# Optimization experiments

Measured on AMD Instinct MI355X. Metric: run time of the kernel, lower is better.

Reference implementation:

```python
import jax, jax.numpy as jnp
import numpy as np

NUM_CLASSES = 2
BG_PID = 5532
NUM_ROIS = 128          # cfg.TRAIN.BATCH_SIZE
NUM_FG_MAX = 32         # round(cfg.TRAIN.FG_FRACTION * BATCH_SIZE), FG_FRACTION = 0.25
FG_THRESH = 0.5
BG_THRESH_HI = 0.5
BG_THRESH_LO = 0.1
MEANS = jnp.array([0.0, 0.0, 0.0, 0.0], dtype=jnp.float32)
STDS = jnp.array([0.1, 0.1, 0.2, 0.2], dtype=jnp.float32)
INSIDE_W = jnp.array([1.0, 1.0, 1.0, 1.0], dtype=jnp.float32)


def _make_boxes(key, n, img_w=1000.0, img_h=600.0):
    k1, k2, k3, k4 = jax.random.split(key, 4)
    x1 = jax.random.uniform(k1, (n,)) * (img_w - 330.0)
    y1 = jax.random.uniform(k2, (n,)) * (img_h - 350.0)
    w = 20.0 + jax.random.uniform(k3, (n,)) * 300.0
    h = 40.0 + jax.random.uniform(k4, (n,)) * 300.0
    return jnp.stack([x1, y1, x1 + w, y1 + h], axis=1).astype(jnp.float32)


def setup_inputs() -> dict:
    key = jax.random.key(0)
    kr, kg, kp = jax.random.split(key, 3)
    R, G = 131072, 256
    rois = _make_boxes(kr, R)
    all_rois = jnp.concatenate([jnp.zeros((R, 1), jnp.float32), rois], axis=1)  # [R,5]
    gtb = _make_boxes(kg, G)
    labels = jnp.ones((G, 1), jnp.float32)  # person class = 1
    pids = jax.random.randint(kp, (G, 1), 0, BG_PID).astype(jnp.float32)
    gt_boxes = jnp.concatenate([gtb, labels, pids], axis=1)  # [G,6]
    return {"all_rois": all_rois, "gt_boxes": gt_boxes}


def bbox_overlaps(a, b):
    iw = jnp.minimum(a[:, None, 2], b[None, :, 2]) - jnp.maximum(a[:, None, 0], b[None, :, 0]) + 1.0
    ih = jnp.minimum(a[:, None, 3], b[None, :, 3]) - jnp.maximum(a[:, None, 1], b[None, :, 1]) + 1.0
    iw = jnp.maximum(iw, 0.0)
    ih = jnp.maximum(ih, 0.0)
    area_a = (a[:, 2] - a[:, 0] + 1.0) * (a[:, 3] - a[:, 1] + 1.0)
    area_b = (b[:, 2] - b[:, 0] + 1.0) * (b[:, 3] - b[:, 1] + 1.0)
    inter = iw * ih
    return inter / (area_a[:, None] + area_b[None, :] - inter)


def bbox_transform(ex, gt):
    ew = ex[:, 2] - ex[:, 0] + 1.0
    eh = ex[:, 3] - ex[:, 1] + 1.0
    ecx = ex[:, 0] + 0.5 * ew
    ecy = ex[:, 1] + 0.5 * eh
    gw = gt[:, 2] - gt[:, 0] + 1.0
    gh = gt[:, 3] - gt[:, 1] + 1.0
    gcx = gt[:, 0] + 0.5 * gw
    gcy = gt[:, 1] + 0.5 * gh
    return jnp.stack([(gcx - ecx) / ew, (gcy - ecy) / eh,
                      jnp.log(gw / ew), jnp.log(gh / eh)], axis=1)


def _forward(all_rois, gt_boxes):
    G = gt_boxes.shape[0]
    gt_rois = jnp.concatenate([jnp.zeros((G, 1), all_rois.dtype), gt_boxes[:, :4]], axis=1)
    rois_all = jnp.concatenate([all_rois, gt_rois], axis=0)  # [R+G,5]
    N = rois_all.shape[0]
    overlaps = bbox_overlaps(rois_all[:, 1:5], gt_boxes[:, :4])  # [R+G, G]
    argmax_ov = jnp.argmax(overlaps, axis=1)
    max_ov = jnp.max(overlaps, axis=1)
    labels_all = gt_boxes[argmax_ov, 4]
    pids_all = gt_boxes[argmax_ov, 5]
    fg_mask = max_ov >= FG_THRESH
    bg_mask = (max_ov < BG_THRESH_HI) & (max_ov >= BG_THRESH_LO)
    num_fg = jnp.minimum(jnp.int32(NUM_FG_MAX), fg_mask.sum().astype(jnp.int32))
    num_bg = jnp.minimum(jnp.int32(NUM_ROIS) - num_fg, bg_mask.sum().astype(jnp.int32))
    # deterministic 'take first k' selection (DEBUG path of the original),
    # expressed as a fixed-shape scatter: rank within fg/bg -> output slot
    fg_rank = (jnp.cumsum(fg_mask) - 1).astype(jnp.int32)
    bg_rank = (jnp.cumsum(bg_mask) - 1).astype(jnp.int32)
    idx = jnp.arange(N, dtype=jnp.int32)
    pos_fg = jnp.where(fg_mask & (fg_rank < num_fg), fg_rank, jnp.int32(NUM_ROIS))
    pos_bg = jnp.where(bg_mask & (bg_rank < num_bg), num_fg + bg_rank, jnp.int32(NUM_ROIS))
    keep = jnp.zeros((NUM_ROIS,), jnp.int32)
    keep = keep.at[pos_fg].set(idx, mode="drop")
    keep = keep.at[pos_bg].set(idx, mode="drop")
    slot_is_fg = jnp.arange(NUM_ROIS) < num_fg
    rois = rois_all[keep]                                   # [128,5]
    labels = jnp.where(slot_is_fg, labels_all[keep], 0.0)
    pids = jnp.where(slot_is_fg, pids_all[keep], jnp.float32(BG_PID))
    tgt = bbox_transform(rois[:, 1:5], gt_boxes[argmax_ov[keep], :4])
    tgt = (tgt - MEANS) / STDS
    cls = jnp.round(labels).astype(jnp.int32)
    onehot = jax.nn.one_hot(cls, NUM_CLASSES, dtype=tgt.dtype) * (labels > 0).astype(tgt.dtype)[:, None]
    bbox_targets = (onehot[:, :, None] * tgt[:, None, :]).reshape(NUM_ROIS, 4 * NUM_CLASSES)
    bbox_inside = (onehot[:, :, None] * INSIDE_W[None, None, :]).reshape(NUM_ROIS, 4 * NUM_CLASSES)
    bbox_outside = (onehot[:, :, None] * jnp.ones((4,), tgt.dtype)).reshape(NUM_ROIS, 4 * NUM_CLASSES)
    return rois, labels, pids, bbox_targets, bbox_inside, bbox_outside


def reference(all_rois, gt_boxes):
    rois, labels, pids, bt, bi, bo = _forward(all_rois, gt_boxes)
    return rois, labels.astype(jnp.int32), pids.astype(jnp.int32), bt, bi, bo
```

## Files before the change

kernel.cpp:

```cpp
#include <hip/hip_runtime.h>
#include <stdint.h>

#define OUT_ROIS 128
#define FG_MAX 32
#define BG_PID_F 5532.0f
#define MAXCH 2304


__global__ __launch_bounds__(256, 4) void ptl_classify(
    const float* __restrict__ all_rois, const float* __restrict__ gt,
    int R, int G, int N,
    ulonglong2* __restrict__ mb2)
{
#pragma clang fp contract(off)
    __shared__ float4 g4[256];
    __shared__ float  gA[256];
    __shared__ uint8_t flg[4][128];
    const int t = threadIdx.x;
    const int w = t >> 6, lane = t & 63;

    if (t < G) {
        const float* p = gt + (size_t)t * 6;
        const float a = p[0], b = p[1], c = p[2], d = p[3];
        g4[t] = make_float4(a, b, c, d);
        gA[t] = ((c - a) + 1.0f) * ((d - b) + 1.0f);
    }
    __syncthreads();

    const int base = blockIdx.x * 128;
    float x1a, y1a, x2a, y2a, x1b, y1b, x2b, y2b;
    {
        const int i0 = base + lane;
        if (i0 < N) {
            if (i0 < R) { const float* p = all_rois + (size_t)i0 * 5; x1a=p[1]; y1a=p[2]; x2a=p[3]; y2a=p[4]; }
            else        { const float* p = gt + (size_t)(i0 - R) * 6; x1a=p[0]; y1a=p[1]; x2a=p[2]; y2a=p[3]; }
        } else { x1a=0.0f; y1a=0.0f; x2a=-2.0f; y2a=-2.0f; }
        const int i1 = base + 64 + lane;
        if (i1 < N) {
            if (i1 < R) { const float* p = all_rois + (size_t)i1 * 5; x1b=p[1]; y1b=p[2]; x2b=p[3]; y2b=p[4]; }
            else        { const float* p = gt + (size_t)(i1 - R) * 6; x1b=p[0]; y1b=p[1]; x2b=p[2]; y2b=p[3]; }
        } else { x1b=0.0f; y1b=0.0f; x2b=-2.0f; y2b=-2.0f; }
    }
    const float Aa = ((x2a - x1a) + 1.0f) * ((y2a - y1a) + 1.0f);
    const float Ab = ((x2b - x1b) + 1.0f) * ((y2b - y1b) + 1.0f);

    float aF0 = -1e38f, aB0 = -1e38f, aF1 = -1e38f, aB1 = -1e38f;

#define IOU2(QQ, GAv)                                                   \
    do {                                                                \
        const float4 q_ = (QQ); const float ga_ = (GAv);                \
        {   float iw = (fminf(x2a, q_.z) - fmaxf(x1a, q_.x)) + 1.0f;    \
            float ih = (fminf(y2a, q_.w) - fmaxf(y1a, q_.y)) + 1.0f;    \
            iw = fmaxf(iw, 0.0f); ih = fmaxf(ih, 0.0f);                 \
            const float I = iw * ih;                                    \
            const float D = (Aa + ga_) - I;                             \
            const float h  = fmaf(-0.5f, D, I);                         \
            const float gF = fmaf(0x1p-26f, D, h);                      \
            const float h2 = fmaf(-0.1f, D, I);                         \
            const float gB = fmaf(0x1p-28f, D, h2);                     \
            aF0 = fmaxf(aF0, gF); aB0 = fmaxf(aB0, gB); }               \
        {   float iw = (fminf(x2b, q_.z) - fmaxf(x1b, q_.x)) + 1.0f;    \
            float ih = (fminf(y2b, q_.w) - fmaxf(y1b, q_.y)) + 1.0f;    \
            iw = fmaxf(iw, 0.0f); ih = fmaxf(ih, 0.0f);                 \
            const float I = iw * ih;                                    \
            const float D = (Ab + ga_) - I;                             \
            const float h  = fmaf(-0.5f, D, I);                         \
            const float gF = fmaf(0x1p-26f, D, h);                      \
            const float h2 = fmaf(-0.1f, D, I);                         \
            const float gB = fmaf(0x1p-28f, D, h2);                     \
            aF1 = fmaxf(aF1, gF); aB1 = fmaxf(aB1, gB); }               \
    } while (0)

    if (G == 256) {
        const int jbeg = w * 64;
        float4 qb0[8], qb1[8];
        float  ga0[8], ga1[8];
#pragma unroll
        for (int uu = 0; uu < 8; ++uu) { qb0[uu] = g4[jbeg + uu]; ga0[uu] = gA[jbeg + uu]; }
#pragma unroll
        for (int grp = 0; grp < 8; ++grp) {
            if ((grp & 1) == 0) {
                if (grp + 1 < 8) {
#pragma unroll
                    for (int uu = 0; uu < 8; ++uu) {
                        qb1[uu] = g4[jbeg + (grp + 1) * 8 + uu];
                        ga1[uu] = gA[jbeg + (grp + 1) * 8 + uu];
                    }
                }
#pragma unroll
                for (int uu = 0; uu < 8; ++uu) IOU2(qb0[uu], ga0[uu]);
            } else {
                if (grp + 1 < 8) {
#pragma unroll
                    for (int uu = 0; uu < 8; ++uu) {
                        qb0[uu] = g4[jbeg + (grp + 1) * 8 + uu];
                        ga0[uu] = gA[jbeg + (grp + 1) * 8 + uu];
                    }
                }
#pragma unroll
                for (int uu = 0; uu < 8; ++uu) IOU2(qb1[uu], ga1[uu]);
            }
        }
    } else {
        const int jbeg = (G * w) >> 2, jend = (G * (w + 1)) >> 2;
        for (int j = jbeg; j < jend; ++j) IOU2(g4[j], gA[j]);
    }
#undef IOU2

    flg[w][lane]      = (uint8_t)((aF0 >= 0.0f ? 1u : 0u) | (aB0 > 0.0f ? 2u : 0u));
    flg[w][64 + lane] = (uint8_t)((aF1 >= 0.0f ? 1u : 0u) | (aB1 > 0.0f ? 2u : 0u));
    __syncthreads();

    if (t < 128) {
        const uint32_t u = (uint32_t)flg[0][t] | flg[1][t] | flg[2][t] | flg[3][t];
        const int i2 = base + t;
        int cls = (u & 1u) ? 1 : ((u & 2u) ? 2 : 0);
        if (i2 >= N) cls = 0;
        unsigned long long mF = __ballot(cls == 1);
        unsigned long long mB = __ballot(cls == 2);
        if ((t & 63) == 0) {
            ulonglong2 v; v.x = mF; v.y = mB;
            mb2[blockIdx.x * 2 + (t >> 6)] = v;
        }
    }
}

__global__ __launch_bounds__(256) void ptl_select_emit(
    const float* __restrict__ all_rois, const float* __restrict__ gt,
    const ulonglong2* __restrict__ mb2,
    int R, int G, int N, int nch,
    float* __restrict__ out)
{
#pragma clang fp contract(off)
    __shared__ int sF[MAXCH], sB[MAXCH];
    __shared__ int tsF[256], tsB[256];
    __shared__ int keep[OUT_ROIS];
    __shared__ int sam[OUT_ROIS];
    __shared__ int nwork;
    __shared__ uint32_t work[256];
    __shared__ float4 g4s[256];
    __shared__ float  gAs[256];
    const int t = threadIdx.x;

    if (t < G) {
        const float* p = gt + (size_t)t * 6;
        const float a = p[0], b = p[1], c = p[2], d = p[3];
        g4s[t] = make_float4(a, b, c, d);
        gAs[t] = ((c - a) + 1.0f) * ((d - b) + 1.0f);
    }
    for (int c = t; c < MAXCH; c += 256) {
        if (c < nch) {
            const ulonglong2 v = mb2[c];
            sF[c] = __popcll(v.x); sB[c] = __popcll(v.y);
        } else { sF[c] = 0; sB[c] = 0; }
    }
    if (t < OUT_ROIS) { keep[t] = 0; sam[t] = 0; }
    if (t == 0) nwork = 0;
    __syncthreads();

    const int c0 = t * (MAXCH / 256);
    int baseF = 0, baseB = 0;
#pragma unroll
    for (int k = 0; k < MAXCH / 256; ++k) { baseF += sF[c0 + k]; baseB += sB[c0 + k]; }
    tsF[t] = baseF; tsB[t] = baseB;
    __syncthreads();
    for (int d = 1; d < 256; d <<= 1) {
        int vF = (t >= d) ? tsF[t - d] : 0;
        int vB = (t >= d) ? tsB[t - d] : 0;
        __syncthreads();
        tsF[t] += vF; tsB[t] += vB;
        __syncthreads();
    }
    const int tf = tsF[255], tb = tsB[255];
    const int num_fg = tf < FG_MAX ? tf : FG_MAX;
    const int rem = OUT_ROIS - num_fg;
    const int num_bg = tb < rem ? tb : rem;

    int rF = tsF[t] - baseF, rB = tsB[t] - baseB;
#pragma unroll
    for (int k = 0; k < MAXCH / 256; ++k) {
        const int c = c0 + k;
        const int cf = sF[c], cb = sB[c];
        const bool need = ((cf > 0 && rF < num_fg) || (cb > 0 && rB < num_bg)) && (c < nch);
        if (need) {
            const uint32_t efc = (uint32_t)(rF < 255 ? rF : 255);
            const uint32_t ebc = (uint32_t)(rB < 255 ? rB : 255);
            const int p = atomicAdd(&nwork, 1);
            work[p] = ((uint32_t)c << 16) | (efc << 8) | ebc;
        }
        rF += cf; rB += cb;
    }
    __syncthreads();

    const int nw = nwork;
    for (int idx = t; idx < nw; idx += 256) {
        const uint32_t e = work[idx];
        const int c = (int)(e >> 16);
        const ulonglong2 v = mb2[c];
        unsigned long long m = v.x;
        int off = (int)((e >> 8) & 0xFF);
        while (m) {
            const int b = __builtin_ctzll(m);
            m &= m - 1;
            if (off < num_fg) keep[off] = c * 64 + b;
            ++off;
        }
        m = v.y;
        off = (int)(e & 0xFF);
        while (m) {
            const int b = __builtin_ctzll(m);
            m &= m - 1;
            if (off < num_bg) keep[num_fg + off] = c * 64 + b;
            ++off;
        }
    }
    __syncthreads();

    {
        const int grp = t >> 3, l8 = t & 7;
        if (grp < num_fg) {
            const int k = keep[grp];
            float x1, y1, x2, y2;
            if (k < R) { const float* p = all_rois + (size_t)k * 5; x1=p[1]; y1=p[2]; x2=p[3]; y2=p[4]; }
            else       { const float* p = gt + (size_t)(k - R) * 6; x1=p[0]; y1=p[1]; x2=p[2]; y2=p[3]; }
            const float A = ((x2 - x1) + 1.0f) * ((y2 - y1) + 1.0f);
            float mv = -1.0f; int mj = 0;
            for (int j = l8; j < G; j += 8) {
                const float4 q = g4s[j];
                const float ga = gAs[j];
                float iw = (fminf(x2, q.z) - fmaxf(x1, q.x)) + 1.0f;
                float ih = (fminf(y2, q.w) - fmaxf(y1, q.y)) + 1.0f;
                iw = fmaxf(iw, 0.0f); ih = fmaxf(ih, 0.0f);
                const float inter = iw * ih;
                const float iou = inter / ((A + ga) - inter);
                if (iou > mv) { mv = iou; mj = j; }
            }
#pragma unroll
            for (int m = 1; m < 8; m <<= 1) {
                const float ov = __shfl_xor(mv, m);
                const int oj = __shfl_xor(mj, m);
                if (ov > mv || (ov == mv && oj < mj)) { mv = ov; mj = oj; }
            }
            if (l8 == 0) sam[grp] = mj;
        }
    }
    __syncthreads();

    if (t < OUT_ROIS) {
        const int s = t;
        const int k = keep[s];
        const bool isfg = s < num_fg;
        float x1, y1, x2, y2;
        if (k < R) { const float* p = all_rois + (size_t)k * 5; x1=p[1]; y1=p[2]; x2=p[3]; y2=p[4]; }
        else       { const float* p = gt + (size_t)(k - R) * 6; x1=p[0]; y1=p[1]; x2=p[2]; y2=p[3]; }
        const int amax = sam[s];
        const float* g = gt + (size_t)amax * 6;
        const float gx1v = g[0], gy1v = g[1], gx2v = g[2], gy2v = g[3];
        const float label = isfg ? g[4] : 0.0f;
        const float pid = isfg ? g[5] : BG_PID_F;

        float* ro = out + (size_t)s * 5;
        ro[0] = 0.0f; ro[1] = x1; ro[2] = y1; ro[3] = x2; ro[4] = y2;
        out[640 + s] = (float)(int)label;
        out[768 + s] = (float)(int)pid;

        const float ew = (x2 - x1) + 1.0f, eh = (y2 - y1) + 1.0f;
        const float ecx = x1 + 0.5f * ew, ecy = y1 + 0.5f * eh;
        const float gw = (gx2v - gx1v) + 1.0f, gh = (gy2v - gy1v) + 1.0f;
        const float gcx = gx1v + 0.5f * gw, gcy = gy1v + 0.5f * gh;
        float tv[4];
        tv[0] = ((gcx - ecx) / ew) / 0.1f;
        tv[1] = ((gcy - ecy) / eh) / 0.1f;
        tv[2] = logf(gw / ew) / 0.2f;
        tv[3] = logf(gh / eh) / 0.2f;

        const int cls = (int)roundf(label);
        const float on = (label > 0.0f) ? 1.0f : 0.0f;

        float* bt = out + 896  + (size_t)s * 8;
        float* bi = out + 1920 + (size_t)s * 8;
        float* bo = out + 2944 + (size_t)s * 8;
#pragma unroll
        for (int cc = 0; cc < 2; ++cc) {
            const float sel = (cc == cls) ? on : 0.0f;
#pragma unroll
            for (int j = 0; j < 4; ++j) {
                bt[cc * 4 + j] = sel * tv[j];
                bi[cc * 4 + j] = sel;
                bo[cc * 4 + j] = sel;
            }
        }
    }
}

extern "C" void kernel_launch(void* const* d_in, const int* in_sizes, int n_in,
                              void* d_out, int out_size, void* d_ws, size_t ws_size,
                              hipStream_t stream) {
    const float* all_rois = (const float*)d_in[0];
    const float* gt       = (const float*)d_in[1];
    const int R = in_sizes[0] / 5;
    const int G = in_sizes[1] / 6;
    const int N = R + G;
    const int nblk = (N + 127) / 128;
    const int nch = (N + 63) / 64;

    ulonglong2* mb2 = (ulonglong2*)d_ws;
    float* out = (float*)d_out;

    ptl_classify<<<nblk, 256, 0, stream>>>(all_rois, gt, R, G, N, mb2);
    ptl_select_emit<<<1, 256, 0, stream>>>(all_rois, gt, mb2, R, G, N, nch, out);
}
```

Measured before the change: 38.74 us.

## Replace shared-memory block scan with register wave-shuffle scan; recompute gt areas inline

The select kernel now keeps per-thread chunk popcounts in registers and computes the prefix sum with wave-level shuffle-up scans plus a four-entry cross-wave combine, replacing the shared-memory staging and the Hillis-Steele block scan that needed many __syncthreads. The classify kernel drops the shared gt-area array and recomputes each gt box area inline from the float4, trading extra ALU work in the hot IoU loop for fewer LDS loads and less shared memory. The inline area is computed in the same order as before, so results should match bitwise.

```diff
diff --git a/kernel.cpp b/kernel.cpp
--- a/kernel.cpp
+++ b/kernel.cpp
@@ -5,6 +5,7 @@
 #define FG_MAX 32
 #define BG_PID_F 5532.0f
 #define MAXCH 2304
+#define CPT 9
 
 
 __global__ __launch_bounds__(256, 4) void ptl_classify(
@@ -14,16 +15,13 @@
 {
 #pragma clang fp contract(off)
     __shared__ float4 g4[256];
-    __shared__ float  gA[256];
     __shared__ uint8_t flg[4][128];
     const int t = threadIdx.x;
     const int w = t >> 6, lane = t & 63;
 
     if (t < G) {
         const float* p = gt + (size_t)t * 6;
-        const float a = p[0], b = p[1], c = p[2], d = p[3];
-        g4[t] = make_float4(a, b, c, d);
-        gA[t] = ((c - a) + 1.0f) * ((d - b) + 1.0f);
+        g4[t] = make_float4(p[0], p[1], p[2], p[3]);
     }
     __syncthreads();
 
@@ -46,9 +44,10 @@
 
     float aF0 = -1e38f, aB0 = -1e38f, aF1 = -1e38f, aB1 = -1e38f;
 
-#define IOU2(QQ, GAv)                                                   \
+#define IOU2(QQ)                                                        \
     do {                                                                \
-        const float4 q_ = (QQ); const float ga_ = (GAv);                \
+        const float4 q_ = (QQ);                                         \
+        const float ga_ = ((q_.z - q_.x) + 1.0f) * ((q_.w - q_.y) + 1.0f); \
         {   float iw = (fminf(x2a, q_.z) - fmaxf(x1a, q_.x)) + 1.0f;    \
             float ih = (fminf(y2a, q_.w) - fmaxf(y1a, q_.y)) + 1.0f;    \
             iw = fmaxf(iw, 0.0f); ih = fmaxf(ih, 0.0f);                 \
@@ -74,36 +73,29 @@
     if (G == 256) {
         const int jbeg = w * 64;
         float4 qb0[8], qb1[8];
-        float  ga0[8], ga1[8];
-#pragma unroll
-        for (int uu = 0; uu < 8; ++uu) { qb0[uu] = g4[jbeg + uu]; ga0[uu] = gA[jbeg + uu]; }
+#pragma unroll
+        for (int uu = 0; uu < 8; ++uu) qb0[uu] = g4[jbeg + uu];
 #pragma unroll
         for (int grp = 0; grp < 8; ++grp) {
             if ((grp & 1) == 0) {
                 if (grp + 1 < 8) {
 #pragma unroll
-                    for (int uu = 0; uu < 8; ++uu) {
-                        qb1[uu] = g4[jbeg + (grp + 1) * 8 + uu];
-                        ga1[uu] = gA[jbeg + (grp + 1) * 8 + uu];
-                    }
+                    for (int uu = 0; uu < 8; ++uu) qb1[uu] = g4[jbeg + (grp + 1) * 8 + uu];
                 }
 #pragma unroll
-                for (int uu = 0; uu < 8; ++uu) IOU2(qb0[uu], ga0[uu]);
+                for (int uu = 0; uu < 8; ++uu) IOU2(qb0[uu]);
             } else {
                 if (grp + 1 < 8) {
 #pragma unroll
-                    for (int uu = 0; uu < 8; ++uu) {
-                        qb0[uu] = g4[jbeg + (grp + 1) * 8 + uu];
-                        ga0[uu] = gA[jbeg + (grp + 1) * 8 + uu];
-                    }
+                    for (int uu = 0; uu < 8; ++uu) qb0[uu] = g4[jbeg + (grp + 1) * 8 + uu];
                 }
 #pragma unroll
-                for (int uu = 0; uu < 8; ++uu) IOU2(qb1[uu], ga1[uu]);
+                for (int uu = 0; uu < 8; ++uu) IOU2(qb1[uu]);
             }
         }
     } else {
         const int jbeg = (G * w) >> 2, jend = (G * (w + 1)) >> 2;
-        for (int j = jbeg; j < jend; ++j) IOU2(g4[j], gA[j]);
+        for (int j = jbeg; j < jend; ++j) IOU2(g4[j]);
     }
 #undef IOU2
 
@@ -132,15 +124,15 @@
     float* __restrict__ out)
 {
 #pragma clang fp contract(off)
-    __shared__ int sF[MAXCH], sB[MAXCH];
-    __shared__ int tsF[256], tsB[256];
+    __shared__ float4 g4s[256];
+    __shared__ float  gAs[256];
     __shared__ int keep[OUT_ROIS];
     __shared__ int sam[OUT_ROIS];
+    __shared__ int wtF[4], wtB[4];
     __shared__ int nwork;
     __shared__ uint32_t work[256];
-    __shared__ float4 g4s[256];
-    __shared__ float  gAs[256];
     const int t = threadIdx.x;
+    const int w = t >> 6, lane = t & 63;
 
     if (t < G) {
         const float* p = gt + (size_t)t * 6;
@@ -148,39 +140,43 @@
         g4s[t] = make_float4(a, b, c, d);
         gAs[t] = ((c - a) + 1.0f) * ((d - b) + 1.0f);
     }
-    for (int c = t; c < MAXCH; c += 256) {
-        if (c < nch) {
-            const ulonglong2 v = mb2[c];
-            sF[c] = __popcll(v.x); sB[c] = __popcll(v.y);
-        } else { sF[c] = 0; sB[c] = 0; }
-    }
     if (t < OUT_ROIS) { keep[t] = 0; sam[t] = 0; }
     if (t == 0) nwork = 0;
-    __syncthreads();
-
-    const int c0 = t * (MAXCH / 256);
-    int baseF = 0, baseB = 0;
-#pragma unroll
-    for (int k = 0; k < MAXCH / 256; ++k) { baseF += sF[c0 + k]; baseB += sB[c0 + k]; }
-    tsF[t] = baseF; tsB[t] = baseB;
-    __syncthreads();
-    for (int d = 1; d < 256; d <<= 1) {
-        int vF = (t >= d) ? tsF[t - d] : 0;
-        int vB = (t >= d) ? tsB[t - d] : 0;
-        __syncthreads();
-        tsF[t] += vF; tsB[t] += vB;
-        __syncthreads();
-    }
-    const int tf = tsF[255], tb = tsB[255];
+
+    int cFr[CPT], cBr[CPT];
+    int sumF = 0, sumB = 0;
+    const int c0 = t * CPT;
+#pragma unroll
+    for (int k = 0; k < CPT; ++k) {
+        int f = 0, b = 0;
+        const int c = c0 + k;
+        if (c < nch) { const ulonglong2 v = mb2[c]; f = __popcll(v.x); b = __popcll(v.y); }
+        cFr[k] = f; cBr[k] = b; sumF += f; sumB += b;
+    }
+    int iF = sumF, iB = sumB;
+#pragma unroll
+    for (int d = 1; d < 64; d <<= 1) {
+        const int vF = __shfl_up(iF, d);
+        const int vB = __shfl_up(iB, d);
+        if (lane >= d) { iF += vF; iB += vB; }
+    }
+    if (lane == 63) { wtF[w] = iF; wtB[w] = iB; }
+    __syncthreads();
+
+    int preF = 0, preB = 0;
+    for (int ww = 0; ww < w; ++ww) { preF += wtF[ww]; preB += wtB[ww]; }
+    const int tf = wtF[0] + wtF[1] + wtF[2] + wtF[3];
+    const int tb = wtB[0] + wtB[1] + wtB[2] + wtB[3];
     const int num_fg = tf < FG_MAX ? tf : FG_MAX;
     const int rem = OUT_ROIS - num_fg;
     const int num_bg = tb < rem ? tb : rem;
 
-    int rF = tsF[t] - baseF, rB = tsB[t] - baseB;
-#pragma unroll
-    for (int k = 0; k < MAXCH / 256; ++k) {
+    int rF = preF + iF - sumF;
+    int rB = preB + iB - sumB;
+#pragma unroll
+    for (int k = 0; k < CPT; ++k) {
         const int c = c0 + k;
-        const int cf = sF[c], cb = sB[c];
+        const int cf = cFr[k], cb = cBr[k];
         const bool need = ((cf > 0 && rF < num_fg) || (cb > 0 && rB < num_bg)) && (c < nch);
         if (need) {
             const uint32_t efc = (uint32_t)(rF < 255 ? rF : 255);
```

Measured after the change: 37.79 us. -2.5%, faster.
